# Kernel tuning notes

Hardware: AMD Instinct MI355X
Metric: run time of the kernel (lower is better)

## Reference

```python
import jax, jax.numpy as jnp
import numpy as np

N_NODES = 100000
N_EDGES = 1000000
D = 64  # input_size == hidden_size
N_CONVS = 6  # order: xz, hz, xr, hr, xh, hh


def setup_inputs() -> dict:
    key = jax.random.key(0)
    ks = jax.random.split(key, 12)
    s = 1.0 / np.sqrt(D)
    inp = {
        "x": jax.random.normal(ks[0], (N_NODES, D), dtype=jnp.float32),
        "h": jax.random.normal(ks[1], (N_NODES, D), dtype=jnp.float32),
        "edge_index": jax.random.randint(ks[2], (2, N_EDGES), 0, N_NODES, dtype=jnp.int32),
        # stacked params for the 6 TransformerConv layers: query/key/value/skip
        "Wq": jax.random.uniform(ks[3], (N_CONVS, D, D), jnp.float32, -s, s),
        "bq": jax.random.uniform(ks[4], (N_CONVS, D), jnp.float32, -s, s),
        "Wk": jax.random.uniform(ks[5], (N_CONVS, D, D), jnp.float32, -s, s),
        "bk": jax.random.uniform(ks[6], (N_CONVS, D), jnp.float32, -s, s),
        "Wv": jax.random.uniform(ks[7], (N_CONVS, D, D), jnp.float32, -s, s),
        "bv": jax.random.uniform(ks[8], (N_CONVS, D), jnp.float32, -s, s),
        "Ws": jax.random.uniform(ks[9], (N_CONVS, D, D), jnp.float32, -s, s),
        "bs": jax.random.uniform(ks[10], (N_CONVS, D), jnp.float32, -s, s),
    }
    return inp


def _transformer_conv(inp, src, dst, Wq, bq, Wk, bk, Wv, bv, Ws, bs):
    # PyG TransformerConv, heads=1, root_weight=True, beta=False
    q = inp @ Wq + bq  # [N, D]
    k = inp @ Wk + bk
    v = inp @ Wv + bv
    scores = jnp.sum(q[dst] * k[src], axis=-1) / jnp.sqrt(jnp.float32(D))  # [E]
    m = jax.ops.segment_max(scores, dst, num_segments=N_NODES)  # [N]
    m = jnp.where(jnp.isfinite(m), m, 0.0)
    e = jnp.exp(scores - m[dst])  # [E]
    denom = jax.ops.segment_sum(e, dst, num_segments=N_NODES)  # [N]
    alpha = e / (denom[dst] + 1e-16)  # [E]
    agg = jax.ops.segment_sum(alpha[:, None] * v[src], dst, num_segments=N_NODES)  # [N, D]
    return agg + inp @ Ws + bs  # skip connection (lin_skip)


def reference(x, h, edge_index, Wq, bq, Wk, bk, Wv, bv, Ws, bs):
    src, dst = edge_index[0], edge_index[1]

    def conv(i, inp):
        return _transformer_conv(inp, src, dst, Wq[i], bq[i], Wk[i], bk[i],
                                 Wv[i], bv[i], Ws[i], bs[i])

    z_g = jax.nn.sigmoid(conv(0, x) + conv(1, h))
    r_g = jax.nn.sigmoid(conv(2, x) + conv(3, h))
    h_tilde = jnp.tanh(conv(4, x) + conv(5, r_g * h))
    return z_g * h + (1.0 - z_g) * h_tilde
```

## Files before the change

### kernel.cpp

```cpp
#include <hip/hip_runtime.h>
#include <math.h>

#define N_NODES 100000
#define N_EDGES 1000000
#define D 64
#define N_CONVS 6
#define CAP 64
#define NDTOT (N_NODES * D)
#define NPART 8
#define CHUNK 4096

typedef __bf16 bf16x8 __attribute__((ext_vector_type(8)));
typedef float f32x4 __attribute__((ext_vector_type(4)));
typedef float f32x2 __attribute__((ext_vector_type(2)));

static __device__ __forceinline__ float hi2f(unsigned int d) {
    union { unsigned int i; float f; } c; c.i = d & 0xFFFF0000u; return c.f;
}
static __device__ __forceinline__ float lo2f(unsigned int d) {
    union { unsigned int i; float f; } c; c.i = d << 16; return c.f;
}
static __device__ __forceinline__ unsigned short f2bf(float f) {
    union { float f; unsigned int i; } c; c.f = f;
    unsigned int x = c.i;
    unsigned int r = (x + 0x7fffu + ((x >> 16) & 1u)) >> 16;
    return (unsigned short)r;
}


#if __has_builtin(__builtin_amdgcn_cvt_pk_f32_fp8) && __has_builtin(__builtin_amdgcn_cvt_pk_fp8_f32)
#define HW_FP8 1
#endif

#ifndef HW_FP8
static __device__ __forceinline__ float dec1(unsigned int b) {
    union { unsigned int i; float f; } c;
    c.i = ((b & 0x80u) << 24) | ((b & 0x7fu) << 20);
    return c.f * 0x1p+120f;
}
static __device__ __forceinline__ unsigned int enc1(float f) {
    union { float f; unsigned int i; } c; c.f = f;
    unsigned int s = (c.i >> 24) & 0x80u;
    float a = fabsf(f);
    a = fminf(a, 448.0f);
    c.f = a * 0x1p-120f;
    unsigned int u = c.i;
    unsigned int bits = (u + 0x7FFFFu + ((u >> 20) & 1u)) >> 20;
    if (bits > 0x7Eu) bits = 0x7Eu;
    return s | bits;
}
#endif

static __device__ __forceinline__ void dec8(unsigned int lo, unsigned int hi, float* f) {
#ifdef HW_FP8
    f32x2 p0 = __builtin_amdgcn_cvt_pk_f32_fp8(lo, false);
    f32x2 p1 = __builtin_amdgcn_cvt_pk_f32_fp8(lo, true);
    f32x2 p2 = __builtin_amdgcn_cvt_pk_f32_fp8(hi, false);
    f32x2 p3 = __builtin_amdgcn_cvt_pk_f32_fp8(hi, true);
    f[0] = p0[0]; f[1] = p0[1]; f[2] = p1[0]; f[3] = p1[1];
    f[4] = p2[0]; f[5] = p2[1]; f[6] = p3[0]; f[7] = p3[1];
#else
#pragma unroll
    for (int i = 0; i < 4; ++i) f[i] = dec1((lo >> (8 * i)) & 0xFFu);
#pragma unroll
    for (int i = 0; i < 4; ++i) f[4 + i] = dec1((hi >> (8 * i)) & 0xFFu);
#endif
}

static __device__ __forceinline__ unsigned int enc4(float a, float b, float c2, float d) {
#ifdef HW_FP8
    int r = 0;
    r = __builtin_amdgcn_cvt_pk_fp8_f32(a, b, r, false);
    r = __builtin_amdgcn_cvt_pk_fp8_f32(c2, d, r, true);
    return (unsigned int)r;
#else
    return enc1(a) | (enc1(b) << 8) | (enc1(c2) << 16) | (enc1(d) << 24);
#endif
}


__global__ void fill_cap_part(const int* __restrict__ src, const int* __restrict__ dst,
                              int E, int* __restrict__ cnt, int* __restrict__ colIdx) {
    const int part = blockIdx.x & (NPART - 1);
    const int base = (blockIdx.x >> 3) * CHUNK;
    const int lo = part * (N_NODES / NPART);
    const int hi = lo + (N_NODES / NPART);
#pragma unroll
    for (int it = 0; it < CHUNK / 256; ++it) {
        int e = base + it * 256 + (int)threadIdx.x;
        if (e < E) {
            int d = dst[e];
            if (d >= lo && d < hi) {
                int slot = atomicAdd(&cnt[d], 1);
                if (slot < CAP) colIdx[(size_t)d * CAP + slot] = src[e];
            }
        }
    }
}


__global__ void prep_all(const float* __restrict__ x, const float* __restrict__ h,
                         unsigned short* __restrict__ xb, unsigned short* __restrict__ hb,
                         const float* __restrict__ Wq, const float* __restrict__ Wk,
                         const float* __restrict__ Wv, const float* __restrict__ Ws,
                         const float* __restrict__ bq, const float* __restrict__ bk,
                         const float* __restrict__ bv, const float* __restrict__ bs,
                         unsigned short* __restrict__ WT, float* __restrict__ ball,
                         int nCvt) {
    int b = blockIdx.x;
    if (b < nCvt) {
        int i = (b * 256 + threadIdx.x) * 4;
        if (i < NDTOT) {
            float4 fx = *(const float4*)&x[i];
            float4 fh = *(const float4*)&h[i];
            ushort4 ux, uh;
            ux.x = f2bf(fx.x); ux.y = f2bf(fx.y); ux.z = f2bf(fx.z); ux.w = f2bf(fx.w);
            uh.x = f2bf(fh.x); uh.y = f2bf(fh.y); uh.z = f2bf(fh.z); uh.w = f2bf(fh.w);
            *(ushort4*)&xb[i] = ux;
            *(ushort4*)&hb[i] = uh;
        }
    } else {
        int idx = (b - nCvt) * 256 + threadIdx.x;
        if (idx >= N_CONVS * 256 * 64) return;
        int conv = idx >> 14;
        int rem = idx & 16383;
        int n = rem >> 6, kk = rem & 63;
        int mat = n >> 6, c = n & 63;
        const float* W = mat == 0 ? Wq : mat == 1 ? Wk : mat == 2 ? Wv : Ws;
        WT[idx] = f2bf(W[conv * 4096 + kk * 64 + c]);
        if (kk == 0) {
            const float* B = mat == 0 ? bq : mat == 1 ? bk : mat == 2 ? bv : bs;
            ball[conv * 256 + n] = B[conv * 64 + c];
        }
    }
}


__global__ __launch_bounds__(512) void gemm_pair(
    const unsigned short* __restrict__ XA, const unsigned short* __restrict__ XB, int N,
    const unsigned short* __restrict__ WTA, const unsigned short* __restrict__ WTB,
    const float* __restrict__ ballA, const float* __restrict__ ballB,
    unsigned short* __restrict__ qboth, unsigned char* __restrict__ kv8,
    float* __restrict__ sk)
{
    __shared__ __align__(16) unsigned short XLA[64][72];
    __shared__ __align__(16) unsigned short XLB[64][72];
    __shared__ __align__(16) float SKIP[64][68];

    const int tid = threadIdx.x;
    const int base = blockIdx.x * 64;
    const int lane = tid & 63;
    const int wave = tid >> 6;
    const int conv = wave >> 2;
    const int mat = wave & 3;

    {
        int r = tid >> 3, cc = (tid & 7) * 8;
        uint4 va = {0u,0u,0u,0u}, vb = {0u,0u,0u,0u};
        if (base + r < N) {
            va = *(const uint4*)&XA[(size_t)(base + r) * D + cc];
            vb = *(const uint4*)&XB[(size_t)(base + r) * D + cc];
        }
        *(uint4*)&XLA[r][cc] = va;
        *(uint4*)&XLB[r][cc] = vb;
    }
    __syncthreads();

    const int l15 = lane & 15;
    const int lhi = lane >> 4;
    const int n0 = mat * 64;
    const unsigned short* WT = conv ? WTB : WTA;
    const float* ball = conv ? ballB : ballA;

    bf16x8 Wf[4][2];
#pragma unroll
    for (int ni = 0; ni < 4; ++ni)
#pragma unroll
        for (int ks = 0; ks < 2; ++ks)
            Wf[ni][ks] = *(const bf16x8*)&WT[(size_t)(n0 + ni * 16 + l15) * D + lhi * 8 + ks * 32];

    bf16x8 Xf[4][2];
#pragma unroll
    for (int mi = 0; mi < 4; ++mi)
#pragma unroll
        for (int ks = 0; ks < 2; ++ks)
            Xf[mi][ks] = conv ? *(const bf16x8*)&XLB[mi * 16 + l15][lhi * 8 + ks * 32]
                              : *(const bf16x8*)&XLA[mi * 16 + l15][lhi * 8 + ks * 32];

    f32x4 acc[4][4];
#pragma unroll
    for (int ni = 0; ni < 4; ++ni) {
        const float4 b4 = *(const float4*)&ball[n0 + ni * 16 + lhi * 4];
#pragma unroll
        for (int mi = 0; mi < 4; ++mi) {
            f32x4 t;
            t[0] = b4.x; t[1] = b4.y; t[2] = b4.z; t[3] = b4.w;
            acc[mi][ni] = t;
        }
    }

#pragma unroll
    for (int ks = 0; ks < 2; ++ks)
#pragma unroll
        for (int mi = 0; mi < 4; ++mi)
#pragma unroll
            for (int ni = 0; ni < 4; ++ni)
                acc[mi][ni] = __builtin_amdgcn_mfma_f32_16x16x32_bf16(
                    Wf[ni][ks], Xf[mi][ks], acc[mi][ni], 0, 0, 0);

    if (mat == 0) {
        unsigned short* outb = qboth + conv * 64;
#pragma unroll
        for (int mi = 0; mi < 4; ++mi) {
            int row = base + mi * 16 + l15;
            if (row < N) {
#pragma unroll
                for (int ni = 0; ni < 4; ++ni) {
                    int col = ni * 16 + lhi * 4;
                    ushort4 u;
                    u.x = f2bf(acc[mi][ni][0]); u.y = f2bf(acc[mi][ni][1]);
                    u.z = f2bf(acc[mi][ni][2]); u.w = f2bf(acc[mi][ni][3]);
                    *(ushort4*)&outb[(size_t)row * 128 + col] = u;
                }
            }
        }
    } else if (mat < 3) {
        unsigned char* outb = kv8 + conv * 128 + (mat == 2 ? 64 : 0);
#pragma unroll
        for (int mi = 0; mi < 4; ++mi) {
            int row = base + mi * 16 + l15;
            if (row < N) {
#pragma unroll
                for (int ni = 0; ni < 4; ++ni) {
                    int col = ni * 16 + lhi * 4;
                    unsigned int r = enc4(acc[mi][ni][0], acc[mi][ni][1],
                                          acc[mi][ni][2], acc[mi][ni][3]);
                    *(unsigned int*)&outb[(size_t)row * 256 + col] = r;
                }
            }
        }
    } else if (conv == 0) {
#pragma unroll
        for (int mi = 0; mi < 4; ++mi)
#pragma unroll
            for (int ni = 0; ni < 4; ++ni)
                *(f32x4*)&SKIP[mi * 16 + l15][ni * 16 + lhi * 4] = acc[mi][ni];
    }
    __syncthreads();
    if (mat == 3 && conv == 1) {
#pragma unroll
        for (int mi = 0; mi < 4; ++mi) {
            int row = base + mi * 16 + l15;
            if (row < N) {
#pragma unroll
                for (int ni = 0; ni < 4; ++ni) {
                    int col = ni * 16 + lhi * 4;
                    const f32x4 s4 = *(const f32x4*)&SKIP[mi * 16 + l15][col];
                    float4 r4;
                    r4.x = acc[mi][ni][0] + s4[0];
                    r4.y = acc[mi][ni][1] + s4[1];
                    r4.z = acc[mi][ni][2] + s4[2];
                    r4.w = acc[mi][ni][3] + s4[3];
                    *(float4*)&sk[(size_t)row * 64 + col] = r4;
                }
            }
        }
    }
}


template<int MODE>
__global__ __launch_bounds__(256) void edge_attn_t(
    const int* __restrict__ cnt, const int* __restrict__ colIdx,
    const unsigned short* __restrict__ qptr,
    const unsigned char* __restrict__ kv8,
    const float* __restrict__ skip, const float* __restrict__ zpre,
    const float* __restrict__ hfull,
    float* __restrict__ tgt, unsigned short* __restrict__ rhb, int N)
{
    const int tid = threadIdx.x;
    const int node = blockIdx.x * 32 + (tid >> 3);
    if (node >= N) return;
    const int t = tid & 7;

    int deg = cnt[node];
    if (deg > CAP) deg = CAP;

    const float SC = 0.18033688f;
    const uint4 qa4 = *(const uint4*)&qptr[(size_t)node * 128 + t * 8];
    const uint4 qb4 = *(const uint4*)&qptr[(size_t)node * 128 + 64 + t * 8];
    float qa[8], qb[8];
    qa[0] = lo2f(qa4.x) * SC; qa[1] = hi2f(qa4.x) * SC;
    qa[2] = lo2f(qa4.y) * SC; qa[3] = hi2f(qa4.y) * SC;
    qa[4] = lo2f(qa4.z) * SC; qa[5] = hi2f(qa4.z) * SC;
    qa[6] = lo2f(qa4.w) * SC; qa[7] = hi2f(qa4.w) * SC;
    qb[0] = lo2f(qb4.x) * SC; qb[1] = hi2f(qb4.x) * SC;
    qb[2] = lo2f(qb4.y) * SC; qb[3] = hi2f(qb4.y) * SC;
    qb[4] = lo2f(qb4.z) * SC; qb[5] = hi2f(qb4.z) * SC;
    qb[6] = lo2f(qb4.w) * SC; qb[7] = hi2f(qb4.w) * SC;

    const size_t rowbase = (size_t)node * CAP;

    float l0 = 0.0f, l1 = 0.0f;
    float a0[8], a1[8];
#pragma unroll
    for (int i = 0; i < 8; ++i) { a0[i] = 0.0f; a1[i] = 0.0f; }

    for (int j = 0; j < deg; j += 2) {
        const bool v2 = (j + 1) < deg;
        const int s1 = colIdx[rowbase + j];
        const int s2 = colIdx[rowbase + (v2 ? j + 1 : j)];
        const unsigned char* p1 = kv8 + (size_t)s1 * 256 + t * 8;
        const unsigned char* p2 = kv8 + (size_t)s2 * 256 + t * 8;
        const uint2 ka1 = *(const uint2*)p1;
        const uint2 va1 = *(const uint2*)(p1 + 64);
        const uint2 kb1 = *(const uint2*)(p1 + 128);
        const uint2 vb1 = *(const uint2*)(p1 + 192);
        const uint2 ka2 = *(const uint2*)p2;
        const uint2 va2 = *(const uint2*)(p2 + 64);
        const uint2 kb2 = *(const uint2*)(p2 + 128);
        const uint2 vb2 = *(const uint2*)(p2 + 192);

        float kf[8];
        dec8(ka1.x, ka1.y, kf);
        float pa1 = qa[0]*kf[0] + qa[1]*kf[1] + qa[2]*kf[2] + qa[3]*kf[3]
                  + qa[4]*kf[4] + qa[5]*kf[5] + qa[6]*kf[6] + qa[7]*kf[7];
        dec8(kb1.x, kb1.y, kf);
        float pb1 = qb[0]*kf[0] + qb[1]*kf[1] + qb[2]*kf[2] + qb[3]*kf[3]
                  + qb[4]*kf[4] + qb[5]*kf[5] + qb[6]*kf[6] + qb[7]*kf[7];
        dec8(ka2.x, ka2.y, kf);
        float pa2 = qa[0]*kf[0] + qa[1]*kf[1] + qa[2]*kf[2] + qa[3]*kf[3]
                  + qa[4]*kf[4] + qa[5]*kf[5] + qa[6]*kf[6] + qa[7]*kf[7];
        dec8(kb2.x, kb2.y, kf);
        float pb2 = qb[0]*kf[0] + qb[1]*kf[1] + qb[2]*kf[2] + qb[3]*kf[3]
                  + qb[4]*kf[4] + qb[5]*kf[5] + qb[6]*kf[6] + qb[7]*kf[7];

        pa1 += __shfl_xor(pa1, 1); pb1 += __shfl_xor(pb1, 1);
        pa2 += __shfl_xor(pa2, 1); pb2 += __shfl_xor(pb2, 1);
        pa1 += __shfl_xor(pa1, 2); pb1 += __shfl_xor(pb1, 2);
        pa2 += __shfl_xor(pa2, 2); pb2 += __shfl_xor(pb2, 2);
        pa1 += __shfl_xor(pa1, 4); pb1 += __shfl_xor(pb1, 4);
        pa2 += __shfl_xor(pa2, 4); pb2 += __shfl_xor(pb2, 4);

        const float w01 = exp2f(pa1);
        const float w11 = exp2f(pb1);
        const float w02 = v2 ? exp2f(pa2) : 0.0f;
        const float w12 = v2 ? exp2f(pb2) : 0.0f;
        l0 += w01 + w02; l1 += w11 + w12;

        float vf1[8], vf2[8];
        dec8(va1.x, va1.y, vf1);
        dec8(va2.x, va2.y, vf2);
#pragma unroll
        for (int i = 0; i < 8; ++i) a0[i] += w01 * vf1[i] + w02 * vf2[i];
        dec8(vb1.x, vb1.y, vf1);
        dec8(vb2.x, vb2.y, vf2);
#pragma unroll
        for (int i = 0; i < 8; ++i) a1[i] += w11 * vf1[i] + w12 * vf2[i];
    }

    const float inv0 = 1.0f / (l0 + 1e-16f);
    const float inv1 = 1.0f / (l1 + 1e-16f);
    float o[8];
#pragma unroll
    for (int i = 0; i < 8; ++i) o[i] = a0[i] * inv0 + a1[i] * inv1;

    const size_t off = (size_t)node * 64 + t * 8;

    if (MODE == 0) {
        float* pout = &tgt[off];
        float4 o1 = *(float4*)pout;
        float4 o2 = *(float4*)(pout + 4);
        o1.x += o[0]; o1.y += o[1]; o1.z += o[2]; o1.w += o[3];
        o2.x += o[4]; o2.y += o[5]; o2.z += o[6]; o2.w += o[7];
        *(float4*)pout = o1;
        *(float4*)(pout + 4) = o2;
    } else if (MODE == 1) {
        const float4 s1 = *(const float4*)&skip[off];
        const float4 s2 = *(const float4*)&skip[off + 4];
        const float4 h1 = *(const float4*)&hfull[off];
        const float4 h2 = *(const float4*)&hfull[off + 4];
        ushort4 u1, u2;
        u1.x = f2bf(h1.x / (1.0f + __expf(-(s1.x + o[0]))));
        u1.y = f2bf(h1.y / (1.0f + __expf(-(s1.y + o[1]))));
        u1.z = f2bf(h1.z / (1.0f + __expf(-(s1.z + o[2]))));
        u1.w = f2bf(h1.w / (1.0f + __expf(-(s1.w + o[3]))));
        u2.x = f2bf(h2.x / (1.0f + __expf(-(s2.x + o[4]))));
        u2.y = f2bf(h2.y / (1.0f + __expf(-(s2.y + o[5]))));
        u2.z = f2bf(h2.z / (1.0f + __expf(-(s2.z + o[6]))));
        u2.w = f2bf(h2.w / (1.0f + __expf(-(s2.w + o[7]))));
        *(ushort4*)&rhb[off] = u1;
        *(ushort4*)&rhb[off + 4] = u2;
    } else {
        const float4 s1 = *(const float4*)&skip[off];
        const float4 s2 = *(const float4*)&skip[off + 4];
        const float4 z1 = *(const float4*)&zpre[off];
        const float4 z2 = *(const float4*)&zpre[off + 4];
        const float4 h1 = *(const float4*)&hfull[off];
        const float4 h2 = *(const float4*)&hfull[off + 4];
        float4 r1, r2;
        float zz;
        zz = 1.0f / (1.0f + __expf(-z1.x)); r1.x = zz * h1.x + (1.0f - zz) * tanhf(s1.x + o[0]);
        zz = 1.0f / (1.0f + __expf(-z1.y)); r1.y = zz * h1.y + (1.0f - zz) * tanhf(s1.y + o[1]);
        zz = 1.0f / (1.0f + __expf(-z1.z)); r1.z = zz * h1.z + (1.0f - zz) * tanhf(s1.z + o[2]);
        zz = 1.0f / (1.0f + __expf(-z1.w)); r1.w = zz * h1.w + (1.0f - zz) * tanhf(s1.w + o[3]);
        zz = 1.0f / (1.0f + __expf(-z2.x)); r2.x = zz * h2.x + (1.0f - zz) * tanhf(s2.x + o[4]);
        zz = 1.0f / (1.0f + __expf(-z2.y)); r2.y = zz * h2.y + (1.0f - zz) * tanhf(s2.y + o[5]);
        zz = 1.0f / (1.0f + __expf(-z2.z)); r2.z = zz * h2.z + (1.0f - zz) * tanhf(s2.z + o[6]);
        zz = 1.0f / (1.0f + __expf(-z2.w)); r2.w = zz * h2.w + (1.0f - zz) * tanhf(s2.w + o[7]);
        *(float4*)&tgt[off] = r1;
        *(float4*)&tgt[off + 4] = r2;
    }
}


extern "C" void kernel_launch(void* const* d_in, const int* in_sizes, int n_in,
                              void* d_out, int out_size, void* d_ws, size_t ws_size,
                              hipStream_t stream) {
    const int N = N_NODES, E = N_EDGES;
    const float* x  = (const float*)d_in[0];
    const float* h  = (const float*)d_in[1];
    const int*  ei  = (const int*)d_in[2];
    const float* Wq = (const float*)d_in[3];
    const float* bq = (const float*)d_in[4];
    const float* Wk = (const float*)d_in[5];
    const float* bk = (const float*)d_in[6];
    const float* Wv = (const float*)d_in[7];
    const float* bv = (const float*)d_in[8];
    const float* Ws = (const float*)d_in[9];
    const float* bs = (const float*)d_in[10];
    float* out = (float*)d_out;

    const int* src = ei;
    const int* dst = ei + E;

    char* w = (char*)d_ws;
    int* cnt    = (int*)w;
    int* colIdx = cnt + N;
    size_t intWords = (size_t)N + (size_t)N * CAP;
    char* p = w + ((intWords * 4 + 255) & ~(size_t)255);

    const size_t ND = (size_t)N * D;
    float* zpre  = (float*)p;            p += ND * 4;
    float* rskip = (float*)p;            p += ND * 4;
    float* ball  = (float*)p;            p += N_CONVS * 256 * 4;
    unsigned short* xb     = (unsigned short*)p; p += ND * 2;
    unsigned short* hb     = (unsigned short*)p; p += ND * 2;
    unsigned short* rhb    = (unsigned short*)p; p += ND * 2;
    unsigned short* qbothA = (unsigned short*)p; p += ND * 2 * 2;
    unsigned short* qbothB = (unsigned short*)p; p += ND * 2 * 2;
    unsigned char*  kv8a   = (unsigned char*)p;  p += (size_t)N_NODES * 256;
    unsigned char*  kv8b   = (unsigned char*)p;  p += (size_t)N_NODES * 256;
    unsigned short* WT     = (unsigned short*)p; p += (size_t)N_CONVS * 256 * 64 * 2;
    float* cskip = rskip;

    const int NB_CVT = (int)(ND / 4 / 256);
    const int NB_PP = (N_CONVS * 256 * 64 + 255) / 256;
    const int NB_GEMM = (N + 63) / 64;
    const int NB_FILL = ((E + CHUNK - 1) / CHUNK) * NPART;
    const int NB_ATTN = (N + 31) / 32;

    prep_all<<<NB_CVT + NB_PP, 256, 0, stream>>>(x, h, xb, hb, Wq, Wk, Wv, Ws,
                                                 bq, bk, bv, bs, WT, ball, NB_CVT);
    hipMemsetAsync(cnt, 0, (size_t)N * sizeof(int), stream);
    fill_cap_part<<<NB_FILL, 256, 0, stream>>>(src, dst, E, cnt, colIdx);

#define WTc(i) (WT + (size_t)(i) * 256 * 64)
#define BLc(i) (ball + (size_t)(i) * 256)

    gemm_pair<<<NB_GEMM, 512, 0, stream>>>(
        xb, hb, N, WTc(0), WTc(1), BLc(0), BLc(1), qbothA, kv8a, zpre);
    gemm_pair<<<NB_GEMM, 512, 0, stream>>>(
        xb, hb, N, WTc(2), WTc(3), BLc(2), BLc(3), qbothB, kv8b, rskip);

    edge_attn_t<0><<<NB_ATTN, 256, 0, stream>>>(
        cnt, colIdx, qbothA, kv8a, nullptr, nullptr, nullptr, zpre, nullptr, N);

    edge_attn_t<1><<<NB_ATTN, 256, 0, stream>>>(
        cnt, colIdx, qbothB, kv8b, rskip, nullptr, h, nullptr, rhb, N);

    gemm_pair<<<NB_GEMM, 512, 0, stream>>>(
        xb, rhb, N, WTc(4), WTc(5), BLc(4), BLc(5), qbothA, kv8a, cskip);

    edge_attn_t<2><<<NB_ATTN, 256, 0, stream>>>(
        cnt, colIdx, qbothA, kv8a, cskip, zpre, h, out, nullptr, N);

#undef WTc
#undef BLc
}
```

Before: 363.9 us.

## Fuse z and r gate GEMMs and edge-attention passes into single launches

```diff
diff --git a/kernel.cpp b/kernel.cpp
--- a/kernel.cpp
+++ b/kernel.cpp
@@ -136,7 +136,8 @@
 }
 
 
-__global__ __launch_bounds__(512) void gemm_pair(
+static __device__ __forceinline__ void gemm_pair_body(
+    int base,
     const unsigned short* __restrict__ XA, const unsigned short* __restrict__ XB, int N,
     const unsigned short* __restrict__ WTA, const unsigned short* __restrict__ WTB,
     const float* __restrict__ ballA, const float* __restrict__ ballB,
@@ -148,7 +149,6 @@
     __shared__ __align__(16) float SKIP[64][68];
 
     const int tid = threadIdx.x;
-    const int base = blockIdx.x * 64;
     const int lane = tid & 63;
     const int wave = tid >> 6;
     const int conv = wave >> 2;
@@ -268,15 +268,158 @@
     }
 }
 
-
-template<int MODE>
-__global__ __launch_bounds__(256) void edge_attn_t(
+__global__ __launch_bounds__(512) void gemm_pair2(
+    const unsigned short* __restrict__ XA, const unsigned short* __restrict__ XB, int N,
+    const unsigned short* __restrict__ WT, const float* __restrict__ ball,
+    unsigned short* __restrict__ qbothA, unsigned short* __restrict__ qbothB,
+    unsigned char* __restrict__ kv8a, unsigned char* __restrict__ kv8b,
+    float* __restrict__ zskip, float* __restrict__ rskip, int NB)
+{
+    const int set = ((int)blockIdx.x >= NB) ? 1 : 0;
+    const int base = ((int)blockIdx.x - set * NB) * 64;
+    gemm_pair_body(base, XA, XB, N,
+                   WT + (size_t)(set * 2) * 256 * 64, WT + (size_t)(set * 2 + 1) * 256 * 64,
+                   ball + (size_t)(set * 2) * 256, ball + (size_t)(set * 2 + 1) * 256,
+                   set ? qbothB : qbothA, set ? kv8b : kv8a,
+                   set ? rskip : zskip);
+}
+
+__global__ __launch_bounds__(512) void gemm_pair(
+    const unsigned short* __restrict__ XA, const unsigned short* __restrict__ XB, int N,
+    const unsigned short* __restrict__ WTA, const unsigned short* __restrict__ WTB,
+    const float* __restrict__ ballA, const float* __restrict__ ballB,
+    unsigned short* __restrict__ qboth, unsigned char* __restrict__ kv8,
+    float* __restrict__ sk)
+{
+    gemm_pair_body((int)blockIdx.x * 64, XA, XB, N, WTA, WTB, ballA, ballB, qboth, kv8, sk);
+}
+
+
+__global__ __launch_bounds__(256) void edge_attn_zr(
     const int* __restrict__ cnt, const int* __restrict__ colIdx,
-    const unsigned short* __restrict__ qptr,
-    const unsigned char* __restrict__ kv8,
-    const float* __restrict__ skip, const float* __restrict__ zpre,
+    const unsigned short* __restrict__ qA, const unsigned short* __restrict__ qB,
+    const unsigned char* __restrict__ kv8a, const unsigned char* __restrict__ kv8b,
+    const float* __restrict__ zskip, const float* __restrict__ rskip,
     const float* __restrict__ hfull,
-    float* __restrict__ tgt, unsigned short* __restrict__ rhb, int N)
+    unsigned short* __restrict__ zb, unsigned short* __restrict__ rhb, int N)
+{
+    const int tid = threadIdx.x;
+    const int node = blockIdx.x * 32 + (tid >> 3);
+    if (node >= N) return;
+    const int t = tid & 7;
+
+    int deg = cnt[node];
+    if (deg > CAP) deg = CAP;
+
+    const float SC = 0.18033688f;
+    float q[4][8];
+    {
+        const uint4 u0 = *(const uint4*)&qA[(size_t)node * 128 + t * 8];
+        const uint4 u1 = *(const uint4*)&qA[(size_t)node * 128 + 64 + t * 8];
+        const uint4 u2 = *(const uint4*)&qB[(size_t)node * 128 + t * 8];
+        const uint4 u3 = *(const uint4*)&qB[(size_t)node * 128 + 64 + t * 8];
+        const uint4 uu[4] = {u0, u1, u2, u3};
+#pragma unroll
+        for (int c = 0; c < 4; ++c) {
+            q[c][0] = lo2f(uu[c].x) * SC; q[c][1] = hi2f(uu[c].x) * SC;
+            q[c][2] = lo2f(uu[c].y) * SC; q[c][3] = hi2f(uu[c].y) * SC;
+            q[c][4] = lo2f(uu[c].z) * SC; q[c][5] = hi2f(uu[c].z) * SC;
+            q[c][6] = lo2f(uu[c].w) * SC; q[c][7] = hi2f(uu[c].w) * SC;
+        }
+    }
+
+    const size_t rowbase = (size_t)node * CAP;
+    float l[4] = {0.0f, 0.0f, 0.0f, 0.0f};
+    float a[4][8];
+#pragma unroll
+    for (int c = 0; c < 4; ++c)
+#pragma unroll
+        for (int i = 0; i < 8; ++i) a[c][i] = 0.0f;
+
+    for (int j = 0; j < deg; ++j) {
+        const int s = colIdx[rowbase + j];
+        const unsigned char* p1 = kv8a + (size_t)s * 256 + t * 8;
+        const unsigned char* p2 = kv8b + (size_t)s * 256 + t * 8;
+        uint2 kk[4], vv[4];
+        kk[0] = *(const uint2*)p1;         vv[0] = *(const uint2*)(p1 + 64);
+        kk[1] = *(const uint2*)(p1 + 128); vv[1] = *(const uint2*)(p1 + 192);
+        kk[2] = *(const uint2*)p2;         vv[2] = *(const uint2*)(p2 + 64);
+        kk[3] = *(const uint2*)(p2 + 128); vv[3] = *(const uint2*)(p2 + 192);
+
+        float pd[4];
+#pragma unroll
+        for (int c = 0; c < 4; ++c) {
+            float kf[8];
+            dec8(kk[c].x, kk[c].y, kf);
+            pd[c] = q[c][0]*kf[0] + q[c][1]*kf[1] + q[c][2]*kf[2] + q[c][3]*kf[3]
+                  + q[c][4]*kf[4] + q[c][5]*kf[5] + q[c][6]*kf[6] + q[c][7]*kf[7];
+        }
+#pragma unroll
+        for (int c = 0; c < 4; ++c) pd[c] += __shfl_xor(pd[c], 1);
+#pragma unroll
+        for (int c = 0; c < 4; ++c) pd[c] += __shfl_xor(pd[c], 2);
+#pragma unroll
+        for (int c = 0; c < 4; ++c) pd[c] += __shfl_xor(pd[c], 4);
+
+#pragma unroll
+        for (int c = 0; c < 4; ++c) {
+            const float wgt = exp2f(pd[c]);
+            l[c] += wgt;
+            float vf[8];
+            dec8(vv[c].x, vv[c].y, vf);
+#pragma unroll
+            for (int i = 0; i < 8; ++i) a[c][i] += wgt * vf[i];
+        }
+    }
+
+    float inv[4];
+#pragma unroll
+    for (int c = 0; c < 4; ++c) inv[c] = 1.0f / (l[c] + 1e-16f);
+
+    const size_t off = (size_t)node * 64 + t * 8;
+    const float4 zs1 = *(const float4*)&zskip[off];
+    const float4 zs2 = *(const float4*)&zskip[off + 4];
+    const float4 rs1 = *(const float4*)&rskip[off];
+    const float4 rs2 = *(const float4*)&rskip[off + 4];
+    const float4 h1 = *(const float4*)&hfull[off];
+    const float4 h2 = *(const float4*)&hfull[off + 4];
+
+    float oz[8], orr[8];
+#pragma unroll
+    for (int i = 0; i < 8; ++i) {
+        oz[i] = a[0][i] * inv[0] + a[1][i] * inv[1];
+        orr[i] = a[2][i] * inv[2] + a[3][i] * inv[3];
+    }
+
+    ushort4 uz1, uz2, ur1, ur2;
+    uz1.x = f2bf(1.0f / (1.0f + __expf(-(zs1.x + oz[0]))));
+    uz1.y = f2bf(1.0f / (1.0f + __expf(-(zs1.y + oz[1]))));
+    uz1.z = f2bf(1.0f / (1.0f + __expf(-(zs1.z + oz[2]))));
+    uz1.w = f2bf(1.0f / (1.0f + __expf(-(zs1.w + oz[3]))));
+    uz2.x = f2bf(1.0f / (1.0f + __expf(-(zs2.x + oz[4]))));
+    uz2.y = f2bf(1.0f / (1.0f + __expf(-(zs2.y + oz[5]))));
+    uz2.z = f2bf(1.0f / (1.0f + __expf(-(zs2.z + oz[6]))));
+    uz2.w = f2bf(1.0f / (1.0f + __expf(-(zs2.w + oz[7]))));
+    ur1.x = f2bf(h1.x / (1.0f + __expf(-(rs1.x + orr[0]))));
+    ur1.y = f2bf(h1.y / (1.0f + __expf(-(rs1.y + orr[1]))));
+    ur1.z = f2bf(h1.z / (1.0f + __expf(-(rs1.z + orr[2]))));
+    ur1.w = f2bf(h1.w / (1.0f + __expf(-(rs1.w + orr[3]))));
+    ur2.x = f2bf(h2.x / (1.0f + __expf(-(rs2.x + orr[4]))));
+    ur2.y = f2bf(h2.y / (1.0f + __expf(-(rs2.y + orr[5]))));
+    ur2.z = f2bf(h2.z / (1.0f + __expf(-(rs2.z + orr[6]))));
+    ur2.w = f2bf(h2.w / (1.0f + __expf(-(rs2.w + orr[7]))));
+    *(ushort4*)&zb[off] = uz1;
+    *(ushort4*)&zb[off + 4] = uz2;
+    *(ushort4*)&rhb[off] = ur1;
+    *(ushort4*)&rhb[off + 4] = ur2;
+}
+
+
+__global__ __launch_bounds__(256) void edge_attn_c(
+    const int* __restrict__ cnt, const int* __restrict__ colIdx,
+    const unsigned short* __restrict__ qptr, const unsigned char* __restrict__ kv8,
+    const float* __restrict__ skip, const unsigned short* __restrict__ zb,
+    const float* __restrict__ hfull, float* __restrict__ out, int N)
 {
     const int tid = threadIdx.x;
     const int node = blockIdx.x * 32 + (tid >> 3);
@@ -300,7 +443,6 @@
     qb[6] = lo2f(qb4.w) * SC; qb[7] = hi2f(qb4.w) * SC;
 
     const size_t rowbase = (size_t)node * CAP;
-
     float l0 = 0.0f, l1 = 0.0f;
     float a0[8], a1[8];
 #pragma unroll
@@ -361,56 +503,34 @@
 
     const float inv0 = 1.0f / (l0 + 1e-16f);
     const float inv1 = 1.0f / (l1 + 1e-16f);
+    const size_t off = (size_t)node * 64 + t * 8;
+
+    const float4 s1 = *(const float4*)&skip[off];
+    const float4 s2 = *(const float4*)&skip[off + 4];
+    const float4 h1 = *(const float4*)&hfull[off];
+    const float4 h2 = *(const float4*)&hfull[off + 4];
+    const uint4 zu = *(const uint4*)&zb[off];
+    float z[8];
+    z[0] = lo2f(zu.x); z[1] = hi2f(zu.x);
+    z[2] = lo2f(zu.y); z[3] = hi2f(zu.y);
+    z[4] = lo2f(zu.z); z[5] = hi2f(zu.z);
+    z[6] = lo2f(zu.w); z[7] = hi2f(zu.w);
+
     float o[8];
 #pragma unroll
     for (int i = 0; i < 8; ++i) o[i] = a0[i] * inv0 + a1[i] * inv1;
 
-    const size_t off = (size_t)node * 64 + t * 8;
-
-    if (MODE == 0) {
-        float* pout = &tgt[off];
-        float4 o1 = *(float4*)pout;
-        float4 o2 = *(float4*)(pout + 4);
-        o1.x += o[0]; o1.y += o[1]; o1.z += o[2]; o1.w += o[3];
-        o2.x += o[4]; o2.y += o[5]; o2.z += o[6]; o2.w += o[7];
-        *(float4*)pout = o1;
-        *(float4*)(pout + 4) = o2;
-    } else if (MODE == 1) {
-        const float4 s1 = *(const float4*)&skip[off];
-        const float4 s2 = *(const float4*)&skip[off + 4];
-        const float4 h1 = *(const float4*)&hfull[off];
-        const float4 h2 = *(const float4*)&hfull[off + 4];
-        ushort4 u1, u2;
-        u1.x = f2bf(h1.x / (1.0f + __expf(-(s1.x + o[0]))));
-        u1.y = f2bf(h1.y / (1.0f + __expf(-(s1.y + o[1]))));
-        u1.z = f2bf(h1.z / (1.0f + __expf(-(s1.z + o[2]))));
-        u1.w = f2bf(h1.w / (1.0f + __expf(-(s1.w + o[3]))));
-        u2.x = f2bf(h2.x / (1.0f + __expf(-(s2.x + o[4]))));
-        u2.y = f2bf(h2.y / (1.0f + __expf(-(s2.y + o[5]))));
-        u2.z = f2bf(h2.z / (1.0f + __expf(-(s2.z + o[6]))));
-        u2.w = f2bf(h2.w / (1.0f + __expf(-(s2.w + o[7]))));
-        *(ushort4*)&rhb[off] = u1;
-        *(ushort4*)&rhb[off + 4] = u2;
-    } else {
-        const float4 s1 = *(const float4*)&skip[off];
-        const float4 s2 = *(const float4*)&skip[off + 4];
-        const float4 z1 = *(const float4*)&zpre[off];
-        const float4 z2 = *(const float4*)&zpre[off + 4];
-        const float4 h1 = *(const float4*)&hfull[off];
-        const float4 h2 = *(const float4*)&hfull[off + 4];
-        float4 r1, r2;
-        float zz;
-        zz = 1.0f / (1.0f + __expf(-z1.x)); r1.x = zz * h1.x + (1.0f - zz) * tanhf(s1.x + o[0]);
-        zz = 1.0f / (1.0f + __expf(-z1.y)); r1.y = zz * h1.y + (1.0f - zz) * tanhf(s1.y + o[1]);
-        zz = 1.0f / (1.0f + __expf(-z1.z)); r1.z = zz * h1.z + (1.0f - zz) * tanhf(s1.z + o[2]);
-        zz = 1.0f / (1.0f + __expf(-z1.w)); r1.w = zz * h1.w + (1.0f - zz) * tanhf(s1.w + o[3]);
-        zz = 1.0f / (1.0f + __expf(-z2.x)); r2.x = zz * h2.x + (1.0f - zz) * tanhf(s2.x + o[4]);
-        zz = 1.0f / (1.0f + __expf(-z2.y)); r2.y = zz * h2.y + (1.0f - zz) * tanhf(s2.y + o[5]);
-        zz = 1.0f / (1.0f + __expf(-z2.z)); r2.z = zz * h2.z + (1.0f - zz) * tanhf(s2.z + o[6]);
-        zz = 1.0f / (1.0f + __expf(-z2.w)); r2.w = zz * h2.w + (1.0f - zz) * tanhf(s2.w + o[7]);
-        *(float4*)&tgt[off] = r1;
-        *(float4*)&tgt[off + 4] = r2;
-    }
+    float4 r1, r2;
+    r1.x = z[0] * h1.x + (1.0f - z[0]) * tanhf(s1.x + o[0]);
+    r1.y = z[1] * h1.y + (1.0f - z[1]) * tanhf(s1.y + o[1]);
+    r1.z = z[2] * h1.z + (1.0f - z[2]) * tanhf(s1.z + o[2]);
+    r1.w = z[3] * h1.w + (1.0f - z[3]) * tanhf(s1.w + o[3]);
+    r2.x = z[4] * h2.x + (1.0f - z[4]) * tanhf(s2.x + o[4]);
+    r2.y = z[5] * h2.y + (1.0f - z[5]) * tanhf(s2.y + o[5]);
+    r2.z = z[6] * h2.z + (1.0f - z[6]) * tanhf(s2.z + o[6]);
+    r2.w = z[7] * h2.w + (1.0f - z[7]) * tanhf(s2.w + o[7]);
+    *(float4*)&out[off] = r1;
+    *(float4*)&out[off + 4] = r2;
 }
 
 
@@ -441,12 +561,13 @@
     char* p = w + ((intWords * 4 + 255) & ~(size_t)255);
 
     const size_t ND = (size_t)N * D;
-    float* zpre  = (float*)p;            p += ND * 4;
+    float* zskip = (float*)p;            p += ND * 4;
     float* rskip = (float*)p;            p += ND * 4;
     float* ball  = (float*)p;            p += N_CONVS * 256 * 4;
     unsigned short* xb     = (unsigned short*)p; p += ND * 2;
     unsigned short* hb     = (unsigned short*)p; p += ND * 2;
     unsigned short* rhb    = (unsigned short*)p; p += ND * 2;
+    unsigned short* zb     = (unsigned short*)p; p += ND * 2;
     unsigned short* qbothA = (unsigned short*)p; p += ND * 2 * 2;
     unsigned short* qbothB = (unsigned short*)p; p += ND * 2 * 2;
     unsigned char*  kv8a   = (unsigned char*)p;  p += (size_t)N_NODES * 256;
@@ -468,22 +589,17 @@
 #define WTc(i) (WT + (size_t)(i) * 256 * 64)
 #define BLc(i) (ball + (size_t)(i) * 256)
 
-    gemm_pair<<<NB_GEMM, 512, 0, stream>>>(
-        xb, hb, N, WTc(0), WTc(1), BLc(0), BLc(1), qbothA, kv8a, zpre);
-    gemm_pair<<<NB_GEMM, 512, 0, stream>>>(
-        xb, hb, N, WTc(2), WTc(3), BLc(2), BLc(3), qbothB, kv8b, rskip);
-
-    edge_attn_t<0><<<NB_ATTN, 256, 0, stream>>>(
-        cnt, colIdx, qbothA, kv8a, nullptr, nullptr, nullptr, zpre, nullptr, N);
-
-    edge_attn_t<1><<<NB_ATTN, 256, 0, stream>>>(
-        cnt, colIdx, qbothB, kv8b, rskip, nullptr, h, nullptr, rhb, N);
+    gemm_pair2<<<2 * NB_GEMM, 512, 0, stream>>>(
+        xb, hb, N, WT, ball, qbothA, qbothB, kv8a, kv8b, zskip, rskip, NB_GEMM);
+
+    edge_attn_zr<<<NB_ATTN, 256, 0, stream>>>(
+        cnt, colIdx, qbothA, qbothB, kv8a, kv8b, zskip, rskip, h, zb, rhb, N);
 
     gemm_pair<<<NB_GEMM, 512, 0, stream>>>(
         xb, rhb, N, WTc(4), WTc(5), BLc(4), BLc(5), qbothA, kv8a, cskip);
 
-    edge_attn_t<2><<<NB_ATTN, 256, 0, stream>>>(
-        cnt, colIdx, qbothA, kv8a, cskip, zpre, h, out, nullptr, N);
+    edge_attn_c<<<NB_ATTN, 256, 0, stream>>>(
+        cnt, colIdx, qbothA, kv8a, cskip, zb, h, out, N);
 
 #undef WTc
 #undef BLc
```

Result: slower. 388.2 us (+6.7%).
